# Optimization experiments

Hardware: AMD Instinct MI355X
Metric: run time of the kernel (lower is better)

The kernel has to match this reference:

```python
import jax, jax.numpy as jnp
import numpy as np

Q_HEADS = 32
KV_HEADS = 8
HEAD_DIM = 64
D_MODEL = 2048
BATCH = 1
SEQ = 2048


def setup_inputs() -> dict:
    key = jax.random.key(0)
    ks = jax.random.split(key, 6)
    s = 0.02
    return {
        "hidden_states": jax.random.normal(ks[0], (BATCH, SEQ, D_MODEL), jnp.float32),
        "Wq": jax.random.normal(ks[1], (D_MODEL, D_MODEL), jnp.float32) * s,
        "bq": jnp.zeros((D_MODEL,), jnp.float32),
        "Wk": jax.random.normal(ks[2], (HEAD_DIM * KV_HEADS, D_MODEL), jnp.float32) * s,
        "bk": jnp.zeros((HEAD_DIM * KV_HEADS,), jnp.float32),
        "Wv": jax.random.normal(ks[3], (HEAD_DIM * KV_HEADS, D_MODEL), jnp.float32) * s,
        "bv": jnp.zeros((HEAD_DIM * KV_HEADS,), jnp.float32),
        "Wo": jax.random.normal(ks[4], (D_MODEL, D_MODEL), jnp.float32) * s,
    }


def _alibi_bias(n, g, dtype):
    # relative_positions = -|j - i| over (n, n), ALiBi slopes over the g group dim
    pos = jnp.arange(n)
    rel = -jnp.abs(pos[None, :] - pos[:, None]).astype(dtype)  # (n, s)
    slopes = (2.0 ** (-jnp.arange(g, dtype=dtype) / g))  # (g,)
    return slopes[None, :, None, None, None] * rel[None, None, None]  # (1,g,1,n,s)


def reference(hidden_states, Wq, bq, Wk, bk, Wv, bv, Wo):
    b, n, _ = hidden_states.shape
    g = Q_HEADS // KV_HEADS  # head groups
    d = HEAD_DIM
    # projections: (b, n, heads, d) -> (b, heads, n, d)
    q = (hidden_states @ Wq.T + bq).reshape(b, n, Q_HEADS, d).transpose(0, 2, 1, 3)
    k = (hidden_states @ Wk.T + bk).reshape(b, n, KV_HEADS, d).transpose(0, 2, 1, 3)
    v = (hidden_states @ Wv.T + bv).reshape(b, n, KV_HEADS, d).transpose(0, 2, 1, 3)
    # scale query, split q heads (h g) -> g outer-group layout: b g h n d
    q = q / jnp.asarray(d ** 0.5, q.dtype)
    q = q.reshape(b, KV_HEADS, g, n, d).transpose(0, 2, 1, 3, 4)  # (b, g, h, n, d)
    sim = jnp.einsum('bghnd,bhsd->bghns', q, k)
    sim = sim + _alibi_bias(n, g, sim.dtype)
    attn = jax.nn.softmax(sim.astype(jnp.float32), axis=-1).astype(q.dtype)
    out = jnp.einsum('bghns,bhsd->bghnd', attn, v)  # (b, g, h, n, d)
    # b g h n d -> b n (h g) d -> b n (h g d)
    out = out.transpose(0, 3, 2, 1, 4).reshape(b, n, Q_HEADS * d)
    return out @ Wo.T
```

## Files before the change

### kernel.cpp

```cpp
#include <hip/hip_runtime.h>
#include <stdint.h>
#include <stddef.h>


typedef unsigned short bf16_t;
typedef __attribute__((ext_vector_type(8))) short short8;
typedef __attribute__((ext_vector_type(4))) float float4v;

#define SEQ  2048
#define DM   2048
#define QKVN 3072
#define KOFF 2048
#define VOFF 2560
#define NH   32

__device__ __forceinline__ bf16_t f2bf(float f) {
  unsigned int u = __float_as_uint(f);
  u += 0x7FFFu + ((u >> 16) & 1u);
  return (bf16_t)(u >> 16);
}

__device__ __forceinline__ void load_lds16(const bf16_t* g, bf16_t* l) {
  __builtin_amdgcn_global_load_lds(
      (__attribute__((address_space(1))) void*)(bf16_t*)g,
      (__attribute__((address_space(3))) void*)l, 16, 0, 0);
}

__device__ __forceinline__ float4v mfma16(short8 a, short8 b, float4v c) {
  return __builtin_amdgcn_mfma_f32_16x16x32_bf16(a, b, c, 0, 0, 0);
}

__device__ __forceinline__ void conv8(const float* __restrict__ in,
                                      bf16_t* __restrict__ out, int i) {
  float4 a = ((const float4*)in)[i * 2 + 0];
  float4 b = ((const float4*)in)[i * 2 + 1];
  short8 v;
  v[0] = (short)f2bf(a.x); v[1] = (short)f2bf(a.y);
  v[2] = (short)f2bf(a.z); v[3] = (short)f2bf(a.w);
  v[4] = (short)f2bf(b.x); v[5] = (short)f2bf(b.y);
  v[6] = (short)f2bf(b.z); v[7] = (short)f2bf(b.w);
  *(short8*)(out + i * 8) = v;
}

__global__ __launch_bounds__(256)
void prep_kernel(const float* __restrict__ hs, const float* __restrict__ Wq,
                 const float* __restrict__ Wk, const float* __restrict__ Wv,
                 const float* __restrict__ Wo, const float* __restrict__ bq,
                 const float* __restrict__ bk, const float* __restrict__ bv,
                 bf16_t* __restrict__ hs_b, bf16_t* __restrict__ Wcat,
                 bf16_t* __restrict__ Wo_b, float* __restrict__ bcat) {
  int bid = blockIdx.x;
  int tid = threadIdx.x;
  if (bid < 2048) {
    conv8(hs, hs_b, bid * 256 + tid);
  } else if (bid < 4096) {
    conv8(Wq, Wcat, (bid - 2048) * 256 + tid);
  } else if (bid < 4608) {
    conv8(Wk, Wcat + (size_t)KOFF * DM, (bid - 4096) * 256 + tid);
  } else if (bid < 5120) {
    conv8(Wv, Wcat + (size_t)VOFF * DM, (bid - 4608) * 256 + tid);
  } else if (bid < 7168) {
    conv8(Wo, Wo_b, (bid - 5120) * 256 + tid);
  } else {
    int j = (bid - 7168) * 256 + tid;
    if (j < 3072)
      bcat[j] = (j < 2048) ? bq[j] : ((j < 2560) ? bk[j - 2048] : bv[j - 2560]);
  }
}

template<int MODE>
__global__ __launch_bounds__(256)
void gemm_bt_kernel(const bf16_t* __restrict__ A, const bf16_t* __restrict__ B,
                    const float* __restrict__ bias, void* __restrict__ Cout,
                    bf16_t* __restrict__ Vt, int M, int N, int K)
{
  __shared__ __align__(16) bf16_t As[64 * 64];
  __shared__ __align__(16) bf16_t Bs[128 * 64];

  const int tid  = threadIdx.x;
  const int wave = tid >> 6;
  const int lane = tid & 63;
  const int q    = lane >> 4;
  const int r    = lane & 15;
  const int srow = lane >> 3;
  const int sc8  = lane & 7;

  const int m0 = blockIdx.y * 64;
  const int n0 = blockIdx.x * 128;
  const int wm = (wave >> 1) * 32;
  const int wn = (wave & 1) * 64;

  float4v acc[2][4] = {};

  for (int k0 = 0; k0 < K; k0 += 64) {
    #pragma unroll
    for (int t = 0; t < 2; ++t) {
      int rowb = wave * 16 + t * 8;
      int row  = rowb + srow;
      int cg   = sc8 ^ (row & 7);
      load_lds16(A + (size_t)(m0 + row) * K + k0 + cg * 8, &As[rowb * 64]);
    }
    #pragma unroll
    for (int t = 0; t < 4; ++t) {
      int rowb = wave * 32 + t * 8;
      int row  = rowb + srow;
      int cg   = sc8 ^ (row & 7);
      load_lds16(B + (size_t)(n0 + row) * K + k0 + cg * 8, &Bs[rowb * 64]);
    }
    __syncthreads();

    #pragma unroll
    for (int ks = 0; ks < 2; ++ks) {
      short8 af[2], bfr[4];
      #pragma unroll
      for (int i = 0; i < 2; ++i) {
        int m = wm + i * 16 + r;
        af[i] = *(const short8*)&As[m * 64 + (((ks * 4 + q) ^ (m & 7)) * 8)];
      }
      #pragma unroll
      for (int j = 0; j < 4; ++j) {
        int n = wn + j * 16 + r;
        bfr[j] = *(const short8*)&Bs[n * 64 + (((ks * 4 + q) ^ (n & 7)) * 8)];
      }
      #pragma unroll
      for (int mi = 0; mi < 2; ++mi)
        #pragma unroll
        for (int ni = 0; ni < 4; ++ni)
          acc[mi][ni] = mfma16(af[mi], bfr[ni], acc[mi][ni]);
    }
    __syncthreads();
  }

  const bool vregion = (MODE == 1) && (n0 >= VOFF);

  #pragma unroll
  for (int mi = 0; mi < 2; ++mi) {
    #pragma unroll
    for (int ni = 0; ni < 4; ++ni) {
      int col = n0 + wn + ni * 16 + r;
      int rowb = m0 + wm + mi * 16 + q * 4;
      float bv = bias ? bias[col] : 0.0f;
      #pragma unroll
      for (int reg = 0; reg < 4; ++reg) {
        float v = acc[mi][ni][reg] + bv;
        if (MODE == 2) {
          ((float*)Cout)[(size_t)(rowb + reg) * N + col] = v;
        } else if (vregion) {
          Vt[(size_t)(col - VOFF) * M + rowb + reg] = f2bf(v);
        } else {
          ((bf16_t*)Cout)[(size_t)(rowb + reg) * N + col] = f2bf(v);
        }
      }
    }
  }
}

__global__ __launch_bounds__(64)
void attn_kernel(const bf16_t* __restrict__ QKV, const bf16_t* __restrict__ Vt,
                 bf16_t* __restrict__ Om)
{
  __shared__ __align__(16) bf16_t Ks[64 * 64];
  __shared__ __align__(16) bf16_t Vs[64 * 64];
  __shared__ __align__(16) bf16_t Pw[32 * 64];

  const int lane = threadIdx.x;
  const int qh   = lane >> 4;
  const int r    = lane & 15;
  const int srow = lane >> 3;
  const int sc8  = lane & 7;

  const int h  = blockIdx.y;
  const int kv = h >> 2;
  const float nslope = -1.44269504f * __builtin_amdgcn_exp2f(-0.25f * (float)(h & 3));
  const float c1 = 0.125f * 1.44269504f;
  const float mC = -17.3123405f;

  const int q0 = blockIdx.x * 32;

  short8 qf[2][2];
  #pragma unroll
  for (int mt = 0; mt < 2; ++mt)
    #pragma unroll
    for (int ks = 0; ks < 2; ++ks)
      qf[mt][ks] = *(const short8*)(QKV + (size_t)(q0 + mt * 16 + r) * QKVN
                                    + h * 64 + ks * 32 + qh * 8);

  float4v o[2][4] = {};
  float lsum[2] = {0.0f, 0.0f};
  const float qgf[2] = {(float)(q0 + r), (float)(q0 + 16 + r)};

  const int t_lo = (q0 >= 64) ? ((q0 - 64) >> 6) : 0;
  const int t_hi = min(SEQ >> 6, (q0 + 96 + 63) >> 6);

  for (int t = t_lo; t < t_hi; ++t) {
    const int s0 = t << 6;
    #pragma unroll
    for (int tt = 0; tt < 8; ++tt) {
      int rowb = tt * 8;
      int row  = rowb + srow;
      int cg   = sc8 ^ (row & 7);
      load_lds16(QKV + (size_t)(s0 + row) * QKVN + KOFF + kv * 64 + cg * 8,
                 &Ks[rowb * 64]);
      load_lds16(Vt + (size_t)(kv * 64 + row) * SEQ + s0 + cg * 8,
                 &Vs[rowb * 64]);
    }
    __syncthreads();

    float4v sa[4][2];
    #pragma unroll
    for (int nt = 0; nt < 4; ++nt) {
      short8 kf0 = *(const short8*)&Ks[(nt * 16 + r) * 64 + (((0 + qh) ^ (r & 7)) * 8)];
      short8 kf1 = *(const short8*)&Ks[(nt * 16 + r) * 64 + (((4 + qh) ^ (r & 7)) * 8)];
      #pragma unroll
      for (int mt = 0; mt < 2; ++mt) {
        float4v zf = {};
        zf = mfma16(kf0, qf[mt][0], zf);
        zf = mfma16(kf1, qf[mt][1], zf);
        sa[nt][mt] = zf;
      }
    }

    #pragma unroll
    for (int nt = 0; nt < 4; ++nt) {
      float sbf = (float)(s0 + nt * 16 + qh * 4);
      #pragma unroll
      for (int mt = 0; mt < 2; ++mt) {
        float df = sbf - qgf[mt];
        float p0 = __builtin_amdgcn_exp2f(fmaf(c1, sa[nt][mt][0], fmaf(nslope, fabsf(df + 0.0f), mC)));
        float p1 = __builtin_amdgcn_exp2f(fmaf(c1, sa[nt][mt][1], fmaf(nslope, fabsf(df + 1.0f), mC)));
        float p2 = __builtin_amdgcn_exp2f(fmaf(c1, sa[nt][mt][2], fmaf(nslope, fabsf(df + 2.0f), mC)));
        float p3 = __builtin_amdgcn_exp2f(fmaf(c1, sa[nt][mt][3], fmaf(nslope, fabsf(df + 3.0f), mC)));
        lsum[mt] += (p0 + p1) + (p2 + p3);
        unsigned int u0 = __float_as_uint(p0) + 0x8000u;
        unsigned int u1 = __float_as_uint(p1) + 0x8000u;
        unsigned int u2 = __float_as_uint(p2) + 0x8000u;
        unsigned int u3 = __float_as_uint(p3) + 0x8000u;
        uint2 pk;
        pk.x = __builtin_amdgcn_perm(u1, u0, 0x07060302u);
        pk.y = __builtin_amdgcn_perm(u3, u2, 0x07060302u);
        int addr = (mt * 16 + r) * 64 + (((nt * 2 + (qh >> 1)) ^ (r & 7)) * 8) + (qh & 1) * 4;
        *(uint2*)(Pw + addr) = pk;
      }
    }

    __asm__ volatile("s_waitcnt lgkmcnt(0)" ::: "memory");

    short8 pa[2][2];
    #pragma unroll
    for (int mt = 0; mt < 2; ++mt) {
      pa[mt][0] = *(const short8*)&Pw[(mt * 16 + r) * 64 + (((0 + qh) ^ (r & 7)) * 8)];
      pa[mt][1] = *(const short8*)&Pw[(mt * 16 + r) * 64 + (((4 + qh) ^ (r & 7)) * 8)];
    }
    #pragma unroll
    for (int dt = 0; dt < 4; ++dt) {
      short8 vb0 = *(const short8*)&Vs[(dt * 16 + r) * 64 + (((0 + qh) ^ (r & 7)) * 8)];
      short8 vb1 = *(const short8*)&Vs[(dt * 16 + r) * 64 + (((4 + qh) ^ (r & 7)) * 8)];
      #pragma unroll
      for (int mt = 0; mt < 2; ++mt) {
        o[mt][dt] = mfma16(pa[mt][0], vb0, o[mt][dt]);
        o[mt][dt] = mfma16(pa[mt][1], vb1, o[mt][dt]);
      }
    }
    __syncthreads();
  }

  #pragma unroll
  for (int mt = 0; mt < 2; ++mt) {
    float lt = lsum[mt];
    lt += __shfl_xor(lt, 16);
    lt += __shfl_xor(lt, 32);
    #pragma unroll
    for (int reg = 0; reg < 4; ++reg) {
      float li = __shfl(lt, qh * 4 + reg);
      float inv = __builtin_amdgcn_rcpf(li);
      int row = q0 + mt * 16 + qh * 4 + reg;
      #pragma unroll
      for (int dt = 0; dt < 4; ++dt)
        Om[(size_t)row * DM + h * 64 + dt * 16 + r] = f2bf(o[mt][dt][reg] * inv);
    }
  }
}

extern "C" void kernel_launch(void* const* d_in, const int* in_sizes, int n_in,
                              void* d_out, int out_size, void* d_ws, size_t ws_size,
                              hipStream_t stream) {
  const float* hs = (const float*)d_in[0];
  const float* Wq = (const float*)d_in[1];
  const float* bq = (const float*)d_in[2];
  const float* Wk = (const float*)d_in[3];
  const float* bk = (const float*)d_in[4];
  const float* Wv = (const float*)d_in[5];
  const float* bv = (const float*)d_in[6];
  const float* Wo = (const float*)d_in[7];

  char* ws = (char*)d_ws;
  const size_t MB = 1024 * 1024;
  bf16_t* hs_b = (bf16_t*)(ws + 0 * MB);
  bf16_t* Ob   = (bf16_t*)(ws + 0 * MB);
  bf16_t* Wcat = (bf16_t*)(ws + 8 * MB);
  bf16_t* Wo_b = (bf16_t*)(ws + 20 * MB);
  float*  bcat = (float*)(ws + 28 * MB);
  bf16_t* QKVb = (bf16_t*)(ws + 29 * MB);
  bf16_t* Vtb  = (bf16_t*)(ws + 41 * MB);

  prep_kernel<<<7180, 256, 0, stream>>>(hs, Wq, Wk, Wv, Wo, bq, bk, bv,
                                        hs_b, Wcat, Wo_b, bcat);

  gemm_bt_kernel<1><<<dim3(QKVN / 128, SEQ / 64), 256, 0, stream>>>(
      hs_b, Wcat, bcat, QKVb, Vtb, SEQ, QKVN, DM);

  attn_kernel<<<dim3(SEQ / 32, NH), 64, 0, stream>>>(QKVb, Vtb, Ob);

  gemm_bt_kernel<2><<<dim3(DM / 128, SEQ / 64), 256, 0, stream>>>(
      Ob, Wo_b, (const float*)nullptr, d_out, (bf16_t*)nullptr, SEQ, DM, DM);
}
```

Before: 182.5 us.

## Switch GEMM to 32x32x16 MFMA with transposed 128x64 block tiles

Rewrites the bf16 GEMM inner loop to use the 32x32x16 MFMA instruction instead of 16x16x32, so each wave computes a 64x32 sub-tile with two accumulators. The block tile becomes 128 rows by 64 columns, launch grids change to match, and the epilogue maps the 16-register MFMA output layout to rows and columns. The aim is fewer LDS fragment reads per MFMA and higher matrix-core throughput per instruction. The epilogue still writes scalar values with a strided pattern, and the V-transpose region needs n0 aligned to VOFF, which holds with 64-wide column tiles.

```diff
diff --git a/kernel.cpp b/kernel.cpp
--- a/kernel.cpp
+++ b/kernel.cpp
@@ -6,6 +6,7 @@
 typedef unsigned short bf16_t;
 typedef __attribute__((ext_vector_type(8))) short short8;
 typedef __attribute__((ext_vector_type(4))) float float4v;
+typedef __attribute__((ext_vector_type(16))) float float16v;
 
 #define SEQ  2048
 #define DM   2048
@@ -28,6 +29,9 @@
 
 __device__ __forceinline__ float4v mfma16(short8 a, short8 b, float4v c) {
   return __builtin_amdgcn_mfma_f32_16x16x32_bf16(a, b, c, 0, 0, 0);
+}
+__device__ __forceinline__ float16v mfma32(short8 a, short8 b, float16v c) {
+  return __builtin_amdgcn_mfma_f32_32x32x16_bf16(a, b, c, 0, 0, 0);
 }
 
 __device__ __forceinline__ void conv8(const float* __restrict__ in,
@@ -74,82 +78,71 @@
                     const float* __restrict__ bias, void* __restrict__ Cout,
                     bf16_t* __restrict__ Vt, int M, int N, int K)
 {
-  __shared__ __align__(16) bf16_t As[64 * 64];
-  __shared__ __align__(16) bf16_t Bs[128 * 64];
+  __shared__ __align__(16) bf16_t As[128 * 64];
+  __shared__ __align__(16) bf16_t Bs[64 * 64];
 
   const int tid  = threadIdx.x;
   const int wave = tid >> 6;
   const int lane = tid & 63;
-  const int q    = lane >> 4;
-  const int r    = lane & 15;
+  const int l31  = lane & 31;
+  const int kh   = lane >> 5;
   const int srow = lane >> 3;
   const int sc8  = lane & 7;
 
-  const int m0 = blockIdx.y * 64;
-  const int n0 = blockIdx.x * 128;
-  const int wm = (wave >> 1) * 32;
-  const int wn = (wave & 1) * 64;
-
-  float4v acc[2][4] = {};
+  const int m0 = blockIdx.y * 128;
+  const int n0 = blockIdx.x * 64;
+  const int wm = (wave & 1) * 64;
+  const int wn = (wave >> 1) * 32;
+
+  float16v acc[2] = {};
 
   for (int k0 = 0; k0 < K; k0 += 64) {
+    #pragma unroll
+    for (int t = 0; t < 4; ++t) {
+      int rowb = wave * 32 + t * 8;
+      int row  = rowb + srow;
+      int cg   = sc8 ^ (row & 7);
+      load_lds16(A + (size_t)(m0 + row) * K + k0 + cg * 8, &As[rowb * 64]);
+    }
     #pragma unroll
     for (int t = 0; t < 2; ++t) {
       int rowb = wave * 16 + t * 8;
       int row  = rowb + srow;
       int cg   = sc8 ^ (row & 7);
-      load_lds16(A + (size_t)(m0 + row) * K + k0 + cg * 8, &As[rowb * 64]);
-    }
-    #pragma unroll
-    for (int t = 0; t < 4; ++t) {
-      int rowb = wave * 32 + t * 8;
-      int row  = rowb + srow;
-      int cg   = sc8 ^ (row & 7);
       load_lds16(B + (size_t)(n0 + row) * K + k0 + cg * 8, &Bs[rowb * 64]);
     }
     __syncthreads();
 
     #pragma unroll
-    for (int ks = 0; ks < 2; ++ks) {
-      short8 af[2], bfr[4];
-      #pragma unroll
-      for (int i = 0; i < 2; ++i) {
-        int m = wm + i * 16 + r;
-        af[i] = *(const short8*)&As[m * 64 + (((ks * 4 + q) ^ (m & 7)) * 8)];
-      }
-      #pragma unroll
-      for (int j = 0; j < 4; ++j) {
-        int n = wn + j * 16 + r;
-        bfr[j] = *(const short8*)&Bs[n * 64 + (((ks * 4 + q) ^ (n & 7)) * 8)];
-      }
-      #pragma unroll
-      for (int mi = 0; mi < 2; ++mi)
-        #pragma unroll
-        for (int ni = 0; ni < 4; ++ni)
-          acc[mi][ni] = mfma16(af[mi], bfr[ni], acc[mi][ni]);
+    for (int ks = 0; ks < 4; ++ks) {
+      int ma = wm + l31;
+      int mb = wm + 32 + l31;
+      int nb = wn + l31;
+      short8 a0 = *(const short8*)&As[ma * 64 + (((ks * 2 + kh) ^ (ma & 7)) * 8)];
+      short8 a1 = *(const short8*)&As[mb * 64 + (((ks * 2 + kh) ^ (mb & 7)) * 8)];
+      short8 b0 = *(const short8*)&Bs[nb * 64 + (((ks * 2 + kh) ^ (nb & 7)) * 8)];
+      acc[0] = mfma32(a0, b0, acc[0]);
+      acc[1] = mfma32(a1, b0, acc[1]);
     }
     __syncthreads();
   }
 
   const bool vregion = (MODE == 1) && (n0 >= VOFF);
+  const int col = n0 + wn + l31;
+  const float bv = bias ? bias[col] : 0.0f;
 
   #pragma unroll
   for (int mi = 0; mi < 2; ++mi) {
     #pragma unroll
-    for (int ni = 0; ni < 4; ++ni) {
-      int col = n0 + wn + ni * 16 + r;
-      int rowb = m0 + wm + mi * 16 + q * 4;
-      float bv = bias ? bias[col] : 0.0f;
-      #pragma unroll
-      for (int reg = 0; reg < 4; ++reg) {
-        float v = acc[mi][ni][reg] + bv;
-        if (MODE == 2) {
-          ((float*)Cout)[(size_t)(rowb + reg) * N + col] = v;
-        } else if (vregion) {
-          Vt[(size_t)(col - VOFF) * M + rowb + reg] = f2bf(v);
-        } else {
-          ((bf16_t*)Cout)[(size_t)(rowb + reg) * N + col] = f2bf(v);
-        }
+    for (int reg = 0; reg < 16; ++reg) {
+      int row = m0 + wm + mi * 32 + (reg & 3) + 4 * kh + 8 * (reg >> 2);
+      float v = acc[mi][reg] + bv;
+      if (MODE == 2) {
+        ((float*)Cout)[(size_t)row * N + col] = v;
+      } else if (vregion) {
+        Vt[(size_t)(col - VOFF) * M + row] = f2bf(v);
+      } else {
+        ((bf16_t*)Cout)[(size_t)row * N + col] = f2bf(v);
       }
     }
   }
@@ -306,11 +299,11 @@
   prep_kernel<<<7180, 256, 0, stream>>>(hs, Wq, Wk, Wv, Wo, bq, bk, bv,
                                         hs_b, Wcat, Wo_b, bcat);
 
-  gemm_bt_kernel<1><<<dim3(QKVN / 128, SEQ / 64), 256, 0, stream>>>(
+  gemm_bt_kernel<1><<<dim3(QKVN / 64, SEQ / 128), 256, 0, stream>>>(
       hs_b, Wcat, bcat, QKVb, Vtb, SEQ, QKVN, DM);
 
   attn_kernel<<<dim3(SEQ / 32, NH), 64, 0, stream>>>(QKVb, Vtb, Ob);
 
-  gemm_bt_kernel<2><<<dim3(DM / 128, SEQ / 64), 256, 0, stream>>>(
+  gemm_bt_kernel<2><<<dim3(DM / 64, SEQ / 128), 256, 0, stream>>>(
       Ob, Wo_b, (const float*)nullptr, d_out, (bf16_t*)nullptr, SEQ, DM, DM);
 }
```

Result: no change. 186.0 us (+1.9%).
